# Performance work log

Hardware: AMD Instinct MI355X
Metric: run time of the kernel (lower is better)

The kernel has to match this reference:

```python
import jax, jax.numpy as jnp
import numpy as np

N, S, Q, E, H, D, F, L = 512, 90, 90, 256, 8, 32, 1024, 3  # batch, kv_len, q_len, embed, heads, head_dim, ffn, layers
POS_VOCAB = 90


def setup_inputs() -> dict:
    key = jax.random.key(0)
    ks = jax.random.split(key, 16)
    rn = lambda k, shp, s=0.05: (jax.random.normal(k, shp, jnp.float32) * s)
    return dict(
        x=jax.random.normal(ks[0], (N, S, E), jnp.float32),
        q=jax.random.normal(ks[1], (N, Q, E), jnp.float32),
        positions=jax.random.randint(ks[2], (N, S), 0, POS_VOCAB),
        pos_emb=rn(ks[3], (POS_VOCAB, E), 1.0),
        # per-head-dim Q/K/V projections, SHARED across heads (as in the torch module)
        Wq=rn(ks[4], (L, D, D)), Wk=rn(ks[5], (L, D, D)), Wv=rn(ks[6], (L, D, D)),
        Wo=rn(ks[7], (L, E, E)), bo=jnp.zeros((L, E), jnp.float32),
        g1=jnp.ones((L, E), jnp.float32), b1=jnp.zeros((L, E), jnp.float32),
        g2=jnp.ones((L, E), jnp.float32), b2=jnp.zeros((L, E), jnp.float32),
        Wf1=rn(ks[8], (L, E, F)), bf1=jnp.zeros((L, F), jnp.float32),
        Wf2=rn(ks[9], (L, F, E)), bf2=jnp.zeros((L, E), jnp.float32),
        Wc1=rn(ks[10], (E, 8), 0.1), bc1=jnp.zeros((8,), jnp.float32),
        Wc2=rn(ks[11], (8, 8), 0.1), bc2=jnp.zeros((8,), jnp.float32),
        Wc3=rn(ks[12], (8, 2), 0.1), bc3=jnp.zeros((2,), jnp.float32),
    )


def _ln(x, g, b, eps=1e-5):
    m = jnp.mean(x, -1, keepdims=True)
    v = jnp.mean((x - m) ** 2, -1, keepdims=True)
    return (x - m) * jax.lax.rsqrt(v + eps) * g + b


def _attn(v_in, k_in, q_in, Wv, Wk, Wq, Wo, bo):
    n, kl, _ = k_in.shape
    ql = q_in.shape[1]
    v = jnp.einsum('nkhd,de->nkhe', v_in.reshape(n, kl, H, D), Wv)
    k = jnp.einsum('nkhd,de->nkhe', k_in.reshape(n, kl, H, D), Wk)
    qh = jnp.einsum('nqhd,de->nqhe', q_in.reshape(n, ql, H, D), Wq)
    # note: scale is 1/sqrt(embed_size) as in the original, not 1/sqrt(head_dim)
    att = jax.nn.softmax(jnp.einsum('nqhd,nkhd->nhqk', qh, k) / jnp.sqrt(jnp.float32(E)), axis=-1)
    o = jnp.einsum('nhqk,nkhd->nqhd', att, v).reshape(n, ql, E)
    return o @ Wo + bo


def reference(x, q, positions, pos_emb, Wq, Wk, Wv, Wo, bo, g1, b1, g2, b2,
              Wf1, bf1, Wf2, bf2, Wc1, bc1, Wc2, bc2, Wc3, bc3):
    out = x + pos_emb[positions]           # dropout = identity at eval
    for i in range(L):
        a = _attn(out, out, q, Wv[i], Wk[i], Wq[i], Wo[i], bo[i])
        h = _ln(a + q, g1[i], b1[i])       # residual uses the ORIGINAL q every layer
        f = jax.nn.relu(h @ Wf1[i] + bf1[i]) @ Wf2[i] + bf2[i]
        out = _ln(f + h, g2[i], b2[i])
    z = jnp.tanh(out @ Wc1 + bc1)
    z = jnp.tanh(z @ Wc2 + bc2)
    return jax.nn.sigmoid(z @ Wc3 + bc3)   # [N, Q, 2]
```

## Files before the change

### kernel.cpp

```cpp
#include <hip/hip_runtime.h>

typedef __bf16 bf16x8 __attribute__((ext_vector_type(8)));
typedef __bf16 bf16x4 __attribute__((ext_vector_type(4)));
typedef float f32x4 __attribute__((ext_vector_type(4)));
typedef unsigned short u16x8 __attribute__((ext_vector_type(8)));
typedef unsigned short u16x4 __attribute__((ext_vector_type(4)));

__device__ __forceinline__ unsigned short f2b(float f) {
    union { float f; unsigned int u; } v; v.f = f;
    unsigned int r = v.u + 0x7fffu + ((v.u >> 16) & 1u);
    return (unsigned short)(r >> 16);
}
__device__ __forceinline__ float b2f(unsigned short b) {
    union { unsigned int u; float f; } v; v.u = ((unsigned int)b) << 16;
    return v.f;
}

__device__ __forceinline__ void gll16(const unsigned short* g, unsigned short* l) {
    __builtin_amdgcn_global_load_lds(
        (const __attribute__((address_space(1))) unsigned int*)g,
        (__attribute__((address_space(3))) unsigned int*)l, 16, 0, 0);
}

__global__ __launch_bounds__(256) void prep_wfrag(
    const float* __restrict__ W, unsigned short* __restrict__ dst, int K, int NN)
{
    int k0 = blockIdx.x * 32, n0 = blockIdx.y * 16;
    int KS = K >> 5;
    size_t fbase = ((size_t)(n0 >> 4) * KS + (k0 >> 5)) * 512;
    for (int p = threadIdx.x; p < 512; p += 256) {
        int e = p & 7, lane = p >> 3;
        int n = lane & 15, k = ((lane >> 4) << 3) + e;
        dst[fbase + p] = f2b(W[(size_t)(k0 + k) * NN + n0 + n]);
    }
}

__global__ __launch_bounds__(256) void prep_wT(
    const float* __restrict__ Wq, const float* __restrict__ Wk, const float* __restrict__ Wv,
    unsigned short* __restrict__ wT)
{
    int l = blockIdx.x / 3, w = blockIdx.x % 3;
    const float* src = (w == 0 ? Wq : w == 1 ? Wk : Wv) + (size_t)l * 1024;
    unsigned short* dst = wT + ((size_t)l * 3 + w) * 1024;
    float scale = (w == 0) ? 0.0625f : 1.0f;
    int t = threadIdx.x;
    f32x4 v = *(const f32x4*)&src[t * 4];
    int d = (t * 4) >> 5, j0 = (t * 4) & 31;
    #pragma unroll
    for (int e = 0; e < 4; e++)
        dst[(j0 + e) * 32 + d] = f2b(v[e] * scale);
}

__global__ __launch_bounds__(256) void add_posemb_q(
    const float* __restrict__ x, const int* __restrict__ pos,
    const float* __restrict__ pe, const float* __restrict__ q,
    unsigned short* __restrict__ cur, unsigned short* __restrict__ qb)
{
    size_t row = blockIdx.x;
    int t = threadIdx.x;
    int p = pos[row];
    cur[row * 256 + t] = f2b(x[row * 256 + t] + pe[(size_t)p * 256 + t]);
    qb[row * 256 + t] = f2b(q[row * 256 + t]);
}

__global__ __launch_bounds__(384, 2) void attn_kernel(
    const unsigned short* __restrict__ cur, const unsigned short* __restrict__ qb,
    const unsigned short* __restrict__ wT,
    unsigned short* __restrict__ og)
{
    __shared__ __align__(16) unsigned short smem[96 * 104 + 96 * 32];
    unsigned short* qs = smem;
    unsigned short* ks = smem + 96 * 40;
    unsigned short* ps = smem;
    unsigned short* vs = smem + 96 * 104;

    int nh = blockIdx.x;
    int n = nh >> 3, h = nh & 7;
    int tid = threadIdx.x;
    int wave = tid >> 6, lane = tid & 63;
    int lr = lane & 15, lg = lane >> 4;
    int hiw = lane & 1;

    bf16x8 wq[2], wk[2], wv[2];
    #pragma unroll
    for (int ct = 0; ct < 2; ct++) {
        int o = (ct * 16 + lr) * 32 + lg * 8;
        wq[ct] = *(const bf16x8*)&wT[o];
        wk[ct] = *(const bf16x8*)&wT[1024 + o];
        wv[ct] = *(const bf16x8*)&wT[2048 + o];
    }

    {
        int tile = wave;
        int row = tile * 16 + lr;
        bf16x8 aq = {0,0,0,0,0,0,0,0}, ac = {0,0,0,0,0,0,0,0};
        if (row < 90) {
            size_t base = ((size_t)(n * 90 + row)) * 256 + h * 32 + lg * 8;
            aq = *(const bf16x8*)&qb[base];
            ac = *(const bf16x8*)&cur[base];
        }
        f32x4 zz = {0.f, 0.f, 0.f, 0.f};
        #pragma unroll
        for (int ct = 0; ct < 2; ct++) {
            f32x4 qc = __builtin_amdgcn_mfma_f32_16x16x32_bf16(aq, wq[ct], zz, 0, 0, 0);
            f32x4 kc = __builtin_amdgcn_mfma_f32_16x16x32_bf16(ac, wk[ct], zz, 0, 0, 0);
            f32x4 vc = __builtin_amdgcn_mfma_f32_16x16x32_bf16(ac, wv[ct], zz, 0, 0, 0);
            #pragma unroll
            for (int rr = 0; rr < 4; rr++) {
                float oq = __shfl_xor(qc[rr], 1);
                unsigned a16 = f2b(qc[rr]), o16 = f2b(oq);
                unsigned pk = hiw ? (o16 | (a16 << 16)) : (a16 | (o16 << 16));
                if ((rr >> 1) == hiw)
                    *(unsigned*)&qs[(tile * 16 + lg * 4 + rr) * 40 + ct * 16 + (lr & ~1)] = pk;

                float ok = __shfl_xor(kc[rr], 1);
                a16 = f2b(kc[rr]); o16 = f2b(ok);
                pk = hiw ? (o16 | (a16 << 16)) : (a16 | (o16 << 16));
                if ((rr >> 1) == hiw)
                    *(unsigned*)&ks[(tile * 16 + lg * 4 + rr) * 40 + ct * 16 + (lr & ~1)] = pk;

                float ov = __shfl_xor(vc[rr], 1);
                a16 = f2b(vc[rr]); o16 = f2b(ov);
                pk = hiw ? (o16 | (a16 << 16)) : (a16 | (o16 << 16));
                if ((rr >> 1) == hiw)
                    *(unsigned*)&vs[(tile * 4 + lg) * 128 + ct * 64 + rr * 16 + (lr & ~1)] = pk;
            }
        }
    }
    __syncthreads();

    f32x4 c[6];
    {
        bf16x8 aq = *(const bf16x8*)&qs[(wave * 16 + lr) * 40 + lg * 8];
        #pragma unroll
        for (int j = 0; j < 6; j++) {
            bf16x8 bk = *(const bf16x8*)&ks[(j * 16 + lr) * 40 + lg * 8];
            f32x4 z = {0.f, 0.f, 0.f, 0.f};
            c[j] = __builtin_amdgcn_mfma_f32_16x16x32_bf16(aq, bk, z, 0, 0, 0);
        }
    }
    if (lr >= 10) { c[5][0] = -1e30f; c[5][1] = -1e30f; c[5][2] = -1e30f; c[5][3] = -1e30f; }

    #pragma unroll
    for (int rr = 0; rr < 4; rr++) {
        float m = c[0][rr];
        #pragma unroll
        for (int j = 1; j < 6; j++) m = fmaxf(m, c[j][rr]);
        m = fmaxf(m, __shfl_xor(m, 1));
        m = fmaxf(m, __shfl_xor(m, 2));
        m = fmaxf(m, __shfl_xor(m, 4));
        m = fmaxf(m, __shfl_xor(m, 8));
        float sum = 0.f;
        #pragma unroll
        for (int j = 0; j < 6; j++) {
            float e = __expf(c[j][rr] - m);
            c[j][rr] = e;
            sum += e;
        }
        sum += __shfl_xor(sum, 1);
        sum += __shfl_xor(sum, 2);
        sum += __shfl_xor(sum, 4);
        sum += __shfl_xor(sum, 8);
        float inv = 1.f / sum;
        #pragma unroll
        for (int j = 0; j < 6; j++) c[j][rr] *= inv;
    }
    __syncthreads();

    {
        int row_base = wave * 16 + lg * 4;
        #pragma unroll
        for (int j = 0; j < 6; j++) {
            #pragma unroll
            for (int rr = 0; rr < 4; rr++) {
                float oth = __shfl_xor(c[j][rr], 1);
                unsigned int own16 = f2b(c[j][rr]), oth16 = f2b(oth);
                unsigned int pk = hiw ? (oth16 | (own16 << 16)) : (own16 | (oth16 << 16));
                if ((rr >> 1) == hiw)
                    *(unsigned int*)&ps[(row_base + rr) * 104 + j * 16 + (lr & ~1)] = pk;
            }
        }
    }
    __syncthreads();

    {
        unsigned vbase = (unsigned)(size_t)&vs[0];
        f32x4 oc0 = {0.f,0.f,0.f,0.f}, oc1 = {0.f,0.f,0.f,0.f};
        #pragma unroll
        for (int s = 0; s < 3; s++) {
            bf16x8 ap = *(const bf16x8*)&ps[(wave * 16 + lr) * 104 + s * 32 + lg * 8];
            unsigned ta = vbase + (unsigned)((8 * s + 2 * lg) * 256) + (unsigned)(lr * 8);
            bf16x4 b0a, b0b, b1a, b1b;
            asm volatile(
                "ds_read_b64_tr_b16 %0, %4\n\t"
                "ds_read_b64_tr_b16 %1, %4 offset:256\n\t"
                "ds_read_b64_tr_b16 %2, %4 offset:128\n\t"
                "ds_read_b64_tr_b16 %3, %4 offset:384\n\t"
                "s_waitcnt lgkmcnt(0)"
                : "=&v"(b0a), "=&v"(b0b), "=&v"(b1a), "=&v"(b1b)
                : "v"(ta) : "memory");
            __builtin_amdgcn_sched_barrier(0);
            bf16x8 bv0, bv1;
            #pragma unroll
            for (int e = 0; e < 4; e++) {
                bv0[e] = b0a[e]; bv0[4 + e] = b0b[e];
                bv1[e] = b1a[e]; bv1[4 + e] = b1b[e];
            }
            oc0 = __builtin_amdgcn_mfma_f32_16x16x32_bf16(ap, bv0, oc0, 0, 0, 0);
            oc1 = __builtin_amdgcn_mfma_f32_16x16x32_bf16(ap, bv1, oc1, 0, 0, 0);
        }
        #pragma unroll
        for (int rr = 0; rr < 4; rr++) {
            int row = wave * 16 + lg * 4 + rr;
            if (row < 90) {
                size_t base = ((size_t)(n * 90 + row)) * 256 + h * 32;
                og[base + lr]      = f2b(oc0[rr]);
                og[base + 16 + lr] = f2b(oc1[rr]);
            }
        }
    }
}

__global__ __launch_bounds__(256, 2) void wo_ffn_fused(
    const unsigned short* __restrict__ A,
    const unsigned short* __restrict__ WoFl, const float* __restrict__ bo,
    const unsigned short* __restrict__ qb, const float* __restrict__ g1, const float* __restrict__ b1,
    const unsigned short* __restrict__ W1F, const float* __restrict__ bf1,
    const unsigned short* __restrict__ W2F, const float* __restrict__ bf2,
    const float* __restrict__ g2, const float* __restrict__ b2,
    unsigned short* __restrict__ C)
{
    __shared__ __align__(16) unsigned short As[8 * 2048];
    __shared__ __align__(16) unsigned short hs[8 * 2048];
    __shared__ float ssum[64 * 4], ssq[64 * 4];

    int bx = blockIdx.x;
    bx = (bx & 7) * 90 + (bx >> 3);
    int ra0 = bx * 64;

    int tid = threadIdx.x;
    int wave = tid >> 6, lane = tid & 63;
    int wc = wave;
    int lr = lane & 15, lg = lane >> 4;
    int rsub = lane >> 2, sp = lane & 3;

    #pragma unroll
    for (int kw = 0; kw < 8; kw++) {
        int r = wave * 16 + rsub;
        int sl = sp ^ ((r >> 1) & 3);
        gll16(&A[(size_t)(ra0 + r) * 256 + kw * 32 + sl * 8], &As[kw * 2048 + wave * 512]);
    }
    asm volatile("s_waitcnt vmcnt(0)" ::: "memory");
    __builtin_amdgcn_s_barrier();
    __builtin_amdgcn_sched_barrier(0);

    {
        f32x4 acc[4][4];
        #pragma unroll
        for (int i = 0; i < 4; i++)
            #pragma unroll
            for (int j = 0; j < 4; j++)
                acc[i][j] = (f32x4){0.f, 0.f, 0.f, 0.f};

        int nt0 = wc * 4;
        bf16x8 xa[4], xb[4];
        #pragma unroll
        for (int j = 0; j < 4; j++)
            xa[j] = *(const bf16x8*)&WoFl[((size_t)(nt0 + j) * 8 + 0) * 512 + lane * 8];
        #pragma unroll
        for (int k2 = 0; k2 < 8; k2 += 2) {
            if (k2 + 1 < 8) {
                #pragma unroll
                for (int j = 0; j < 4; j++)
                    xb[j] = *(const bf16x8*)&WoFl[((size_t)(nt0 + j) * 8 + k2 + 1) * 512 + lane * 8];
            }
            {
                bf16x8 ya[4];
                #pragma unroll
                for (int i = 0; i < 4; i++) {
                    int mm = i * 16 + lr;
                    ya[i] = *(const bf16x8*)&As[k2 * 2048 + mm * 32 + (lg ^ ((mm >> 1) & 3)) * 8];
                }
                #pragma unroll
                for (int i = 0; i < 4; i++)
                    #pragma unroll
                    for (int j = 0; j < 4; j++)
                        acc[i][j] = __builtin_amdgcn_mfma_f32_16x16x32_bf16(xa[j], ya[i], acc[i][j], 0, 0, 0);
            }
            if (k2 + 2 < 8) {
                #pragma unroll
                for (int j = 0; j < 4; j++)
                    xa[j] = *(const bf16x8*)&WoFl[((size_t)(nt0 + j) * 8 + k2 + 2) * 512 + lane * 8];
            }
            {
                bf16x8 ya[4];
                #pragma unroll
                for (int i = 0; i < 4; i++) {
                    int mm = i * 16 + lr;
                    ya[i] = *(const bf16x8*)&As[(k2 + 1) * 2048 + mm * 32 + (lg ^ ((mm >> 1) & 3)) * 8];
                }
                #pragma unroll
                for (int i = 0; i < 4; i++)
                    #pragma unroll
                    for (int j = 0; j < 4; j++)
                        acc[i][j] = __builtin_amdgcn_mfma_f32_16x16x32_bf16(xb[j], ya[i], acc[i][j], 0, 0, 0);
            }
        }

        float s1[4] = {0.f,0.f,0.f,0.f}, sq[4] = {0.f,0.f,0.f,0.f};
        #pragma unroll
        for (int i = 0; i < 4; i++) {
            int row = ra0 + i * 16 + lr;
            #pragma unroll
            for (int j = 0; j < 4; j++) {
                int ncol = wc * 64 + j * 16 + lg * 4;
                f32x4 bv = *(const f32x4*)&bo[ncol];
                u16x4 rv = *(const u16x4*)&qb[(size_t)row * 256 + ncol];
                #pragma unroll
                for (int rr = 0; rr < 4; rr++) {
                    acc[i][j][rr] += bv[rr] + b2f(rv[rr]);
                    s1[i] += acc[i][j][rr];
                    sq[i] += acc[i][j][rr] * acc[i][j][rr];
                }
            }
        }
        #pragma unroll
        for (int i = 0; i < 4; i++) {
            s1[i] += __shfl_xor(s1[i], 16);  s1[i] += __shfl_xor(s1[i], 32);
            sq[i] += __shfl_xor(sq[i], 16);  sq[i] += __shfl_xor(sq[i], 32);
            if (lg == 0) {
                int rb = i * 16 + lr;
                ssum[rb * 4 + wc] = s1[i];
                ssq[rb * 4 + wc]  = sq[i];
            }
        }
        __syncthreads();
        #pragma unroll
        for (int i = 0; i < 4; i++) {
            int rb = i * 16 + lr;
            float ts = 0.f, tq = 0.f;
            #pragma unroll
            for (int w = 0; w < 4; w++) { ts += ssum[rb * 4 + w]; tq += ssq[rb * 4 + w]; }
            float mean = ts * (1.f / 256.f);
            float var = tq * (1.f / 256.f) - mean * mean;
            float inv = rsqrtf(var + 1e-5f);
            #pragma unroll
            for (int j = 0; j < 4; j++) {
                int ncol = wc * 64 + j * 16 + lg * 4;
                f32x4 gv = *(const f32x4*)&g1[ncol];
                f32x4 bv = *(const f32x4*)&b1[ncol];
                int row = i * 16 + lr;
                int win = ncol >> 5, cw = ncol & 31;
                int p = (cw >> 3) ^ ((row >> 1) & 3);
                u16x4 ov;
                #pragma unroll
                for (int rr = 0; rr < 4; rr++)
                    ov[rr] = f2b((acc[i][j][rr] - mean) * inv * gv[rr] + bv[rr]);
                *(u16x4*)&hs[win * 2048 + row * 32 + p * 8 + (cw & 7)] = ov;
            }
        }
    }
    __syncthreads();

    f32x4 acc2[4][4];
    #pragma unroll
    for (int i = 0; i < 4; i++)
        #pragma unroll
        for (int j = 0; j < 4; j++)
            acc2[i][j] = (f32x4){0.f, 0.f, 0.f, 0.f};

    #pragma unroll 1
    for (int fc = 0; fc < 4; fc++) {
        f32x4 acc1[4][4];
        #pragma unroll
        for (int i = 0; i < 4; i++)
            #pragma unroll
            for (int j = 0; j < 4; j++)
                acc1[i][j] = (f32x4){0.f, 0.f, 0.f, 0.f};

        int ntb1 = fc * 16 + wc * 4;
        bf16x8 xa[4], xb[4];
        #pragma unroll
        for (int j = 0; j < 4; j++)
            xa[j] = *(const bf16x8*)&W1F[((size_t)(ntb1 + j) * 8 + 0) * 512 + lane * 8];
        #pragma unroll
        for (int k2 = 0; k2 < 8; k2 += 2) {
            if (k2 + 1 < 8) {
                #pragma unroll
                for (int j = 0; j < 4; j++)
                    xb[j] = *(const bf16x8*)&W1F[((size_t)(ntb1 + j) * 8 + k2 + 1) * 512 + lane * 8];
            }
            {
                bf16x8 ya[4];
                #pragma unroll
                for (int i = 0; i < 4; i++) {
                    int mm = i * 16 + lr;
                    ya[i] = *(const bf16x8*)&hs[k2 * 2048 + mm * 32 + (lg ^ ((mm >> 1) & 3)) * 8];
                }
                #pragma unroll
                for (int i = 0; i < 4; i++)
                    #pragma unroll
                    for (int j = 0; j < 4; j++)
                        acc1[i][j] = __builtin_amdgcn_mfma_f32_16x16x32_bf16(xa[j], ya[i], acc1[i][j], 0, 0, 0);
            }
            if (k2 + 2 < 8) {
                #pragma unroll
                for (int j = 0; j < 4; j++)
                    xa[j] = *(const bf16x8*)&W1F[((size_t)(ntb1 + j) * 8 + k2 + 2) * 512 + lane * 8];
            }
            {
                bf16x8 ya[4];
                #pragma unroll
                for (int i = 0; i < 4; i++) {
                    int mm = i * 16 + lr;
                    ya[i] = *(const bf16x8*)&hs[(k2 + 1) * 2048 + mm * 32 + (lg ^ ((mm >> 1) & 3)) * 8];
                }
                #pragma unroll
                for (int i = 0; i < 4; i++)
                    #pragma unroll
                    for (int j = 0; j < 4; j++)
                        acc1[i][j] = __builtin_amdgcn_mfma_f32_16x16x32_bf16(xb[j], ya[i], acc1[i][j], 0, 0, 0);
            }
        }

        __syncthreads();
        #pragma unroll
        for (int i = 0; i < 4; i++) {
            int row = i * 16 + lr;
            #pragma unroll
            for (int j = 0; j < 4; j++) {
                int ncol = wc * 64 + j * 16 + lg * 4;
                f32x4 bv = *(const f32x4*)&bf1[fc * 256 + ncol];
                int win = ncol >> 5, cw = ncol & 31;
                int p = (cw >> 3) ^ ((row >> 1) & 3);
                u16x4 ov;
                #pragma unroll
                for (int rr = 0; rr < 4; rr++)
                    ov[rr] = f2b(fmaxf(acc1[i][j][rr] + bv[rr], 0.f));
                *(u16x4*)&As[win * 2048 + row * 32 + p * 8 + (cw & 7)] = ov;
            }
        }
        __syncthreads();

        int ntb2 = wc * 4;
        #pragma unroll
        for (int j = 0; j < 4; j++)
            xa[j] = *(const bf16x8*)&W2F[((size_t)(ntb2 + j) * 32 + fc * 8 + 0) * 512 + lane * 8];
        #pragma unroll
        for (int k2 = 0; k2 < 8; k2 += 2) {
            if (k2 + 1 < 8) {
                #pragma unroll
                for (int j = 0; j < 4; j++)
                    xb[j] = *(const bf16x8*)&W2F[((size_t)(ntb2 + j) * 32 + fc * 8 + k2 + 1) * 512 + lane * 8];
            }
            {
                bf16x8 ya[4];
                #pragma unroll
                for (int i = 0; i < 4; i++) {
                    int mm = i * 16 + lr;
                    ya[i] = *(const bf16x8*)&As[k2 * 2048 + mm * 32 + (lg ^ ((mm >> 1) & 3)) * 8];
                }
                #pragma unroll
                for (int i = 0; i < 4; i++)
                    #pragma unroll
                    for (int j = 0; j < 4; j++)
                        acc2[i][j] = __builtin_amdgcn_mfma_f32_16x16x32_bf16(xa[j], ya[i], acc2[i][j], 0, 0, 0);
            }
            if (k2 + 2 < 8) {
                #pragma unroll
                for (int j = 0; j < 4; j++)
                    xa[j] = *(const bf16x8*)&W2F[((size_t)(ntb2 + j) * 32 + fc * 8 + k2 + 2) * 512 + lane * 8];
            }
            {
                bf16x8 ya[4];
                #pragma unroll
                for (int i = 0; i < 4; i++) {
                    int mm = i * 16 + lr;
                    ya[i] = *(const bf16x8*)&As[(k2 + 1) * 2048 + mm * 32 + (lg ^ ((mm >> 1) & 3)) * 8];
                }
                #pragma unroll
                for (int i = 0; i < 4; i++)
                    #pragma unroll
                    for (int j = 0; j < 4; j++)
                        acc2[i][j] = __builtin_amdgcn_mfma_f32_16x16x32_bf16(xb[j], ya[i], acc2[i][j], 0, 0, 0);
            }
        }
    }
    __syncthreads();

    float s1[4] = {0.f,0.f,0.f,0.f}, sq[4] = {0.f,0.f,0.f,0.f};
    #pragma unroll
    for (int i = 0; i < 4; i++) {
        int row = i * 16 + lr;
        #pragma unroll
        for (int j = 0; j < 4; j++) {
            int ncol = wc * 64 + j * 16 + lg * 4;
            f32x4 bv = *(const f32x4*)&bf2[ncol];
            int win = ncol >> 5, cw = ncol & 31;
            int p = (cw >> 3) ^ ((row >> 1) & 3);
            u16x4 rv = *(const u16x4*)&hs[win * 2048 + row * 32 + p * 8 + (cw & 7)];
            #pragma unroll
            for (int rr = 0; rr < 4; rr++) {
                acc2[i][j][rr] += bv[rr] + b2f(rv[rr]);
                s1[i] += acc2[i][j][rr];
                sq[i] += acc2[i][j][rr] * acc2[i][j][rr];
            }
        }
    }
    #pragma unroll
    for (int i = 0; i < 4; i++) {
        s1[i] += __shfl_xor(s1[i], 16);  s1[i] += __shfl_xor(s1[i], 32);
        sq[i] += __shfl_xor(sq[i], 16);  sq[i] += __shfl_xor(sq[i], 32);
        if (lg == 0) {
            int rb = i * 16 + lr;
            ssum[rb * 4 + wc] = s1[i];
            ssq[rb * 4 + wc]  = sq[i];
        }
    }
    __syncthreads();
    #pragma unroll
    for (int i = 0; i < 4; i++) {
        int rb = i * 16 + lr;
        float ts = 0.f, tq = 0.f;
        #pragma unroll
        for (int w = 0; w < 4; w++) { ts += ssum[rb * 4 + w]; tq += ssq[rb * 4 + w]; }
        float mean = ts * (1.f / 256.f);
        float var = tq * (1.f / 256.f) - mean * mean;
        float inv = rsqrtf(var + 1e-5f);
        int row = ra0 + rb;
        #pragma unroll
        for (int j = 0; j < 4; j++) {
            int ncol = wc * 64 + j * 16 + lg * 4;
            f32x4 gv = *(const f32x4*)&g2[ncol];
            f32x4 bv = *(const f32x4*)&b2[ncol];
            u16x4 ov;
            #pragma unroll
            for (int rr = 0; rr < 4; rr++)
                ov[rr] = f2b((acc2[i][j][rr] - mean) * inv * gv[rr] + bv[rr]);
            *(u16x4*)&C[(size_t)row * 256 + ncol] = ov;
        }
    }
}

__global__ __launch_bounds__(256) void classifier(
    const unsigned short* __restrict__ xin,
    const float* __restrict__ Wc1, const float* __restrict__ bc1,
    const float* __restrict__ Wc2, const float* __restrict__ bc2,
    const float* __restrict__ Wc3, const float* __restrict__ bc3,
    float* __restrict__ out)
{
    __shared__ float w1[256][9];
    __shared__ float w2[64], b2s[8], w3[16], b3s[2], b1s[8];
    int t = threadIdx.x;
    #pragma unroll
    for (int i = 0; i < 8; i++) {
        int idx = t + i * 256;
        w1[idx >> 3][idx & 7] = Wc1[idx];
    }
    if (t < 64) w2[t] = Wc2[t];
    if (t < 16) w3[t] = Wc3[t];
    if (t < 8) { b2s[t] = bc2[t]; b1s[t] = bc1[t]; }
    if (t < 2) b3s[t] = bc3[t];
    __syncthreads();
    int g = t >> 3, m = t & 7;
    size_t row = (size_t)blockIdx.x * 32 + g;
    float z[8] = {0.f,0.f,0.f,0.f,0.f,0.f,0.f,0.f};
    const unsigned short* xr = xin + row * 256 + m * 32;
    #pragma unroll
    for (int cidx = 0; cidx < 4; cidx++) {
        u16x8 xv = *(const u16x8*)&xr[cidx * 8];
        #pragma unroll
        for (int e = 0; e < 8; e++) {
            float xf = b2f(xv[e]);
            int ei = m * 32 + cidx * 8 + e;
            #pragma unroll
            for (int j = 0; j < 8; j++) z[j] = fmaf(xf, w1[ei][j], z[j]);
        }
    }
    #pragma unroll
    for (int d = 1; d < 8; d <<= 1)
        #pragma unroll
        for (int j = 0; j < 8; j++) z[j] += __shfl_xor(z[j], d);
    float z1[8], z2[8];
    #pragma unroll
    for (int j = 0; j < 8; j++) z1[j] = tanhf(z[j] + b1s[j]);
    #pragma unroll
    for (int j2 = 0; j2 < 8; j2++) {
        float sacc = b2s[j2];
        #pragma unroll
        for (int j = 0; j < 8; j++) sacc = fmaf(z1[j], w2[j * 8 + j2], sacc);
        z2[j2] = tanhf(sacc);
    }
    if (m < 2) {
        float sacc = b3s[m];
        #pragma unroll
        for (int j = 0; j < 8; j++) sacc = fmaf(z2[j], w3[j * 2 + m], sacc);
        out[row * 2 + m] = 1.f / (1.f + __expf(-sacc));
    }
}

extern "C" void kernel_launch(void* const* d_in, const int* in_sizes, int n_in,
                              void* d_out, int out_size, void* d_ws, size_t ws_size,
                              hipStream_t stream) {
    const float* x        = (const float*)d_in[0];
    const float* q        = (const float*)d_in[1];
    const int*   positions= (const int*)d_in[2];
    const float* pos_emb  = (const float*)d_in[3];
    const float* Wq       = (const float*)d_in[4];
    const float* Wk       = (const float*)d_in[5];
    const float* Wv       = (const float*)d_in[6];
    const float* Wo       = (const float*)d_in[7];
    const float* bo       = (const float*)d_in[8];
    const float* g1       = (const float*)d_in[9];
    const float* b1       = (const float*)d_in[10];
    const float* g2       = (const float*)d_in[11];
    const float* b2       = (const float*)d_in[12];
    const float* Wf1      = (const float*)d_in[13];
    const float* bf1      = (const float*)d_in[14];
    const float* Wf2      = (const float*)d_in[15];
    const float* bf2      = (const float*)d_in[16];
    const float* Wc1      = (const float*)d_in[17];
    const float* bc1      = (const float*)d_in[18];
    const float* Wc2      = (const float*)d_in[19];
    const float* bc2      = (const float*)d_in[20];
    const float* Wc3      = (const float*)d_in[21];
    const float* bc3      = (const float*)d_in[22];
    float* out = (float*)d_out;

    const int R = 512 * 90;
    char* ws = (char*)d_ws;
    size_t off = 0;
    auto alloc = [&](size_t bytes) -> void* {
        void* p = ws + off;
        off += (bytes + 255) & ~(size_t)255;
        return p;
    };
    unsigned short* cur = (unsigned short*)alloc((size_t)R * 256 * 2);
    unsigned short* qb  = (unsigned short*)alloc((size_t)R * 256 * 2);
    unsigned short* qho = (unsigned short*)alloc((size_t)R * 256 * 2);
    unsigned short* WoF = (unsigned short*)alloc((size_t)3 * 256 * 256 * 2);
    unsigned short* W1F = (unsigned short*)alloc((size_t)3 * 1024 * 256 * 2);
    unsigned short* W2F = (unsigned short*)alloc((size_t)3 * 256 * 1024 * 2);
    unsigned short* WTqkv = (unsigned short*)alloc((size_t)3 * 3 * 1024 * 2);

    for (int l = 0; l < 3; l++) {
        prep_wfrag<<<dim3(8, 16),  256, 0, stream>>>(Wo  + (size_t)l*256*256,  WoF + (size_t)l*256*256,  256, 256);
        prep_wfrag<<<dim3(8, 64),  256, 0, stream>>>(Wf1 + (size_t)l*256*1024, W1F + (size_t)l*1024*256, 256, 1024);
        prep_wfrag<<<dim3(32, 16), 256, 0, stream>>>(Wf2 + (size_t)l*1024*256, W2F + (size_t)l*256*1024, 1024, 256);
    }
    prep_wT<<<9, 256, 0, stream>>>(Wq, Wk, Wv, WTqkv);
    add_posemb_q<<<R, 256, 0, stream>>>(x, positions, pos_emb, q, cur, qb);

    for (int l = 0; l < 3; l++) {
        attn_kernel<<<512 * 8, 384, 0, stream>>>(cur, qb, WTqkv + (size_t)l * 3 * 1024, qho);
        wo_ffn_fused<<<dim3(720), 256, 0, stream>>>(
            qho, WoF + (size_t)l*256*256, bo + l*256,
            qb, g1 + l*256, b1 + l*256,
            W1F + (size_t)l*1024*256, bf1 + l*1024,
            W2F + (size_t)l*256*1024, bf2 + l*256,
            g2 + l*256, b2 + l*256, cur);
    }
    classifier<<<R / 32, 256, 0, stream>>>(cur, Wc1, bc1, Wc2, bc2, Wc3, bc3, out);
}
```

Measured before the change: 463.7 us.

## Keep attention probabilities in registers via transposed QK^T and lane shuffles

```diff
diff --git a/kernel.cpp b/kernel.cpp
--- a/kernel.cpp
+++ b/kernel.cpp
@@ -68,11 +68,9 @@
     const unsigned short* __restrict__ wT,
     unsigned short* __restrict__ og)
 {
-    __shared__ __align__(16) unsigned short smem[96 * 104 + 96 * 32];
-    unsigned short* qs = smem;
-    unsigned short* ks = smem + 96 * 40;
-    unsigned short* ps = smem;
-    unsigned short* vs = smem + 96 * 104;
+    __shared__ __align__(16) unsigned short qs[96 * 40];
+    __shared__ __align__(16) unsigned short ks[96 * 40];
+    __shared__ __align__(16) unsigned short vs[96 * 32];
 
     int nh = blockIdx.x;
     int n = nh >> 3, h = nh & 7;
@@ -129,66 +127,69 @@
     }
     __syncthreads();
 
-    f32x4 c[6];
+    f32x4 cs[6];
     {
         bf16x8 aq = *(const bf16x8*)&qs[(wave * 16 + lr) * 40 + lg * 8];
         #pragma unroll
         for (int j = 0; j < 6; j++) {
             bf16x8 bk = *(const bf16x8*)&ks[(j * 16 + lr) * 40 + lg * 8];
             f32x4 z = {0.f, 0.f, 0.f, 0.f};
-            c[j] = __builtin_amdgcn_mfma_f32_16x16x32_bf16(aq, bk, z, 0, 0, 0);
-        }
-    }
-    if (lr >= 10) { c[5][0] = -1e30f; c[5][1] = -1e30f; c[5][2] = -1e30f; c[5][3] = -1e30f; }
-
-    #pragma unroll
-    for (int rr = 0; rr < 4; rr++) {
-        float m = c[0][rr];
-        #pragma unroll
-        for (int j = 1; j < 6; j++) m = fmaxf(m, c[j][rr]);
-        m = fmaxf(m, __shfl_xor(m, 1));
-        m = fmaxf(m, __shfl_xor(m, 2));
-        m = fmaxf(m, __shfl_xor(m, 4));
-        m = fmaxf(m, __shfl_xor(m, 8));
-        float sum = 0.f;
-        #pragma unroll
-        for (int j = 0; j < 6; j++) {
-            float e = __expf(c[j][rr] - m);
-            c[j][rr] = e;
+            cs[j] = __builtin_amdgcn_mfma_f32_16x16x32_bf16(bk, aq, z, 0, 0, 0);
+        }
+    }
+    #pragma unroll
+    for (int rr = 0; rr < 4; rr++)
+        if (lg * 4 + rr >= 10) cs[5][rr] = -1e30f;
+
+    float mx = cs[0][0];
+    #pragma unroll
+    for (int j = 0; j < 6; j++)
+        #pragma unroll
+        for (int rr = 0; rr < 4; rr++) mx = fmaxf(mx, cs[j][rr]);
+    mx = fmaxf(mx, __shfl_xor(mx, 16));
+    mx = fmaxf(mx, __shfl_xor(mx, 32));
+    float sum = 0.f;
+    #pragma unroll
+    for (int j = 0; j < 6; j++)
+        #pragma unroll
+        for (int rr = 0; rr < 4; rr++) {
+            float e = __expf(cs[j][rr] - mx);
+            cs[j][rr] = e;
             sum += e;
         }
-        sum += __shfl_xor(sum, 1);
-        sum += __shfl_xor(sum, 2);
-        sum += __shfl_xor(sum, 4);
-        sum += __shfl_xor(sum, 8);
-        float inv = 1.f / sum;
-        #pragma unroll
-        for (int j = 0; j < 6; j++) c[j][rr] *= inv;
-    }
-    __syncthreads();
-
-    {
-        int row_base = wave * 16 + lg * 4;
-        #pragma unroll
-        for (int j = 0; j < 6; j++) {
-            #pragma unroll
-            for (int rr = 0; rr < 4; rr++) {
-                float oth = __shfl_xor(c[j][rr], 1);
-                unsigned int own16 = f2b(c[j][rr]), oth16 = f2b(oth);
-                unsigned int pk = hiw ? (oth16 | (own16 << 16)) : (own16 | (oth16 << 16));
-                if ((rr >> 1) == hiw)
-                    *(unsigned int*)&ps[(row_base + rr) * 104 + j * 16 + (lr & ~1)] = pk;
-            }
-        }
-    }
-    __syncthreads();
+    sum += __shfl_xor(sum, 16);
+    sum += __shfl_xor(sum, 32);
+    float inv = 1.f / sum;
+
+    unsigned pk0[6], pk1[6];
+    #pragma unroll
+    for (int j = 0; j < 6; j++) {
+        pk0[j] = (unsigned)f2b(cs[j][0]) | ((unsigned)f2b(cs[j][1]) << 16);
+        pk1[j] = (unsigned)f2b(cs[j][2]) | ((unsigned)f2b(cs[j][3]) << 16);
+    }
 
     {
         unsigned vbase = (unsigned)(size_t)&vs[0];
+        int sel = lg >> 1;
+        int base_lo = lr + ((lg & 1) * 2) * 16;
+        int base_hi = base_lo + 16;
         f32x4 oc0 = {0.f,0.f,0.f,0.f}, oc1 = {0.f,0.f,0.f,0.f};
         #pragma unroll
         for (int s = 0; s < 3; s++) {
-            bf16x8 ap = *(const bf16x8*)&ps[(wave * 16 + lr) * 104 + s * 32 + lg * 8];
+            unsigned A0 = __shfl(pk0[2*s],     base_lo);
+            unsigned A1 = __shfl(pk1[2*s],     base_lo);
+            unsigned B0 = __shfl(pk0[2*s + 1], base_lo);
+            unsigned B1 = __shfl(pk1[2*s + 1], base_lo);
+            unsigned C0 = __shfl(pk0[2*s],     base_hi);
+            unsigned C1 = __shfl(pk1[2*s],     base_hi);
+            unsigned D0 = __shfl(pk0[2*s + 1], base_hi);
+            unsigned D1 = __shfl(pk1[2*s + 1], base_hi);
+            union { unsigned u[4]; bf16x8 v; } apu;
+            apu.u[0] = sel ? B0 : A0;
+            apu.u[1] = sel ? B1 : A1;
+            apu.u[2] = sel ? D0 : C0;
+            apu.u[3] = sel ? D1 : C1;
+
             unsigned ta = vbase + (unsigned)((8 * s + 2 * lg) * 256) + (unsigned)(lr * 8);
             bf16x4 b0a, b0b, b1a, b1b;
             asm volatile(
@@ -206,16 +207,17 @@
                 bv0[e] = b0a[e]; bv0[4 + e] = b0b[e];
                 bv1[e] = b1a[e]; bv1[4 + e] = b1b[e];
             }
-            oc0 = __builtin_amdgcn_mfma_f32_16x16x32_bf16(ap, bv0, oc0, 0, 0, 0);
-            oc1 = __builtin_amdgcn_mfma_f32_16x16x32_bf16(ap, bv1, oc1, 0, 0, 0);
+            oc0 = __builtin_amdgcn_mfma_f32_16x16x32_bf16(apu.v, bv0, oc0, 0, 0, 0);
+            oc1 = __builtin_amdgcn_mfma_f32_16x16x32_bf16(apu.v, bv1, oc1, 0, 0, 0);
         }
         #pragma unroll
         for (int rr = 0; rr < 4; rr++) {
+            float invr = __shfl(inv, lg * 4 + rr);
             int row = wave * 16 + lg * 4 + rr;
             if (row < 90) {
                 size_t base = ((size_t)(n * 90 + row)) * 256 + h * 32;
-                og[base + lr]      = f2b(oc0[rr]);
-                og[base + 16 + lr] = f2b(oc1[rr]);
+                og[base + lr]      = f2b(oc0[rr] * invr);
+                og[base + 16 + lr] = f2b(oc1[rr] * invr);
             }
         }
     }
```

Result: faster. 439.1 us, median of 2 (-5.3%).
